# Performance work log

Measured on AMD Instinct MI355X. Metric: run time of the kernel, lower is better.

The kernel has to match this reference:

```python
import jax, jax.numpy as jnp
import numpy as np

B, D, F = 4096, 2048, 16384


def setup_inputs() -> dict:
    key = jax.random.key(0)
    ks = jax.random.split(key, 5)
    s_enc = 1.0 / np.sqrt(D)
    s_dec = 1.0 / np.sqrt(F)
    return {
        "x": jax.random.normal(ks[0], (B, D), dtype=jnp.float32),
        "W_enc": jax.random.normal(ks[1], (F, D), dtype=jnp.float32) * s_enc,
        "b_enc": jnp.zeros((F,), dtype=jnp.float32),
        "W_kest1": jax.random.normal(ks[2], (F, D), dtype=jnp.float32) * s_enc,
        "b_kest1": jnp.zeros((F,), dtype=jnp.float32),
        "W_kest2": jax.random.normal(ks[3], (1, F), dtype=jnp.float32) * s_dec,
        "b_kest2": jnp.zeros((1,), dtype=jnp.float32),
        "W_dec": jax.random.normal(ks[4], (D, F), dtype=jnp.float32) * s_dec,
        "b_dec": jnp.zeros((D,), dtype=jnp.float32),
        "k": 64,
    }


def topk_per_row(acts, k_est):
    # rank of each element when sorted descending (ties resolved stably;
    # after ReLU ties are zeros, so output is identical either way)
    order = jnp.argsort(-acts, axis=1)          # [B, F] descending order
    rank = jnp.argsort(order, axis=1)           # rank[i,j] = position of acts[i,j]
    mask = rank < k_est[:, None]                # per-row dynamic (float) k
    return acts * mask


def reference(x, W_enc, b_enc, W_kest1, b_kest1, W_kest2, b_kest2, W_dec, b_dec, k):
    xc = x - b_dec                                              # [B, D]
    acts = jax.nn.relu(xc @ W_enc.T + b_enc)                    # [B, F]
    h = jax.nn.relu(xc @ W_kest1.T + b_kest1)                   # [B, F]
    k_est = jax.nn.sigmoid(h @ W_kest2.T + b_kest2)[:, 0] * (2.0 * k)  # [B]
    enc = topk_per_row(acts, k_est)                             # [B, F] sparse codes
    x_hat = enc @ W_dec.T + b_dec                               # [B, D]
    return x_hat
```

## Files before the change

kernel.cpp:

```cpp
#include <hip/hip_runtime.h>
#include <hip/hip_bf16.h>
#include <cstdint>
#include <cstddef>

#define BATCH 4096
#define DIM   2048
#define FEAT  16384
#define MAXF  2048

typedef __attribute__((ext_vector_type(8))) _Float16 h8v;
typedef __attribute__((ext_vector_type(4))) float f4v;
typedef __attribute__((ext_vector_type(4))) unsigned short us4v;

__device__ __forceinline__ void split2(float v, unsigned short &h, unsigned short &l){
  _Float16 hf = (_Float16)v;
  _Float16 lf = (_Float16)((v - (float)hf) * 2048.0f);
  h = __builtin_bit_cast(unsigned short, hf);
  l = __builtin_bit_cast(unsigned short, lf);
}

__device__ __forceinline__ void gload16(const void* g, void* l){
  __builtin_amdgcn_global_load_lds(
      (const __attribute__((address_space(1))) void*)g,
      (__attribute__((address_space(3))) void*)l, 16, 0, 0);
}

__global__ __launch_bounds__(256)
void splitX(const float* __restrict__ x, const float* __restrict__ bdec,
            unsigned short* __restrict__ p0, unsigned short* __restrict__ p1)
{
  const size_t i = ((size_t)blockIdx.x * 256 + threadIdx.x) * 4;
  const int col = (int)(i & (DIM - 1));
  const float4 v = *(const float4*)(x + i);
  const float4 b = *(const float4*)(bdec + col);
  float e0 = v.x - b.x, e1 = v.y - b.y, e2 = v.z - b.z, e3 = v.w - b.w;
  ushort4 H, L;
  split2(e0, H.x, L.x); split2(e1, H.y, L.y);
  split2(e2, H.z, L.z); split2(e3, H.w, L.w);
  *(ushort4*)(p0 + i) = H; *(ushort4*)(p1 + i) = L;
}

__global__ __launch_bounds__(256)
void splitW(const float* __restrict__ w,
            unsigned short* __restrict__ p0, unsigned short* __restrict__ p1)
{
  const size_t i = ((size_t)blockIdx.x * 256 + threadIdx.x) * 4;
  const float4 v = *(const float4*)(w + i);
  ushort4 H, L;
  split2(v.x, H.x, L.x); split2(v.y, H.y, L.y);
  split2(v.z, H.z, L.z); split2(v.w, H.w, L.w);
  *(ushort4*)(p0 + i) = H; *(ushort4*)(p1 + i) = L;
}

__global__ __launch_bounds__(256)
void splitW1(const float* __restrict__ w, unsigned short* __restrict__ p0)
{
  const size_t i = ((size_t)blockIdx.x * 256 + threadIdx.x) * 4;
  const float4 v = *(const float4*)(w + i);
  ushort4 H;
  H.x = __builtin_bit_cast(unsigned short, (_Float16)v.x);
  H.y = __builtin_bit_cast(unsigned short, (_Float16)v.y);
  H.z = __builtin_bit_cast(unsigned short, (_Float16)v.z);
  H.w = __builtin_bit_cast(unsigned short, (_Float16)v.w);
  *(ushort4*)(p0 + i) = H;
}

__global__ __launch_bounds__(256, 2)
void gemmd(const unsigned short* __restrict__ Ah_, const unsigned short* __restrict__ B1h_,
           const unsigned short* __restrict__ B2h_,
           const float* __restrict__ benc, const float* __restrict__ bk1,
           const float* __restrict__ w2,
           _Float16* __restrict__ acts16, float* __restrict__ zpart)
{
  __shared__ unsigned short sAB[2][3][128][32];
  const int tid  = threadIdx.x;
  const int lane = tid & 63, wv = tid >> 6;

  const int bid = blockIdx.x;
  const int xcd = bid & 7;
  const int idx = bid >> 3;
  const int sq  = idx >> 6;
  const int s   = idx & 63;
  const int bx  = (xcd << 4) | ((sq & 1) << 3) | (s & 7);
  const int by  = ((sq >> 1) << 3) | (s >> 3);
  const int row0 = by << 7, col0 = bx << 7;

  const int wr = (wv & 1) << 6, wc = (wv >> 1) << 6;

  f4v acc1[4][4], acc2[4][4];
  #pragma unroll
  for (int i = 0; i < 4; ++i)
    #pragma unroll
    for (int j = 0; j < 4; ++j){
      acc1[i][j] = (f4v){0.f, 0.f, 0.f, 0.f};
      acc2[i][j] = (f4v){0.f, 0.f, 0.f, 0.f};
    }

  const unsigned short* gsrc[6];
  unsigned ldsoff[6];
  #pragma unroll
  for (int j = 0; j < 6; ++j){
    const int q = wv * 6 + j;
    const int mat = q >> 3;
    const int chunk = q & 7;
    const int r  = (chunk << 4) + (lane >> 2);
    const int gl = (lane & 3) ^ ((r >> 1) & 3);
    const int rowg = ((mat == 0) ? row0 : col0) + r;
    const unsigned short* P = (mat == 0) ? Ah_ : ((mat == 1) ? B1h_ : B2h_);
    gsrc[j]  = P + (size_t)rowg * DIM + (gl << 3);
    ldsoff[j] = (unsigned)(mat * 8192 + chunk * 1024);
  }

  const int fr16 = lane & 15;
  const int kg   = lane >> 4;
  int ra[4], rb[4];
  #pragma unroll
  for (int f = 0; f < 4; ++f){ ra[f] = wr + (f << 4) + fr16; rb[f] = wc + (f << 4) + fr16; }

  #define LDFRAGD(bf, mat, r) \
    (*(const h8v*)((const char*)sAB + (bf) * 24576 + (mat) * 8192 + (r) * 64 + (((kg ^ (((r) >> 1) & 3)) << 4))))
  #define STAGED(bf, ko)                                                      \
    {                                                                         \
      _Pragma("unroll")                                                       \
      for (int j = 0; j < 6; ++j)                                             \
        gload16(gsrc[j] + (ko), (char*)sAB + (bf) * 24576 + ldsoff[j]);       \
    }

  int cur = 0;
  STAGED(0, 0);
  __syncthreads();

  for (int kt = 0; kt < DIM / 32; ++kt){
    if (kt < DIM / 32 - 1) STAGED(cur ^ 1, (kt + 1) << 5);

    h8v Ahf[4], Bf[4];
    #pragma unroll
    for (int f = 0; f < 4; ++f) Ahf[f] = LDFRAGD(cur, 0, ra[f]);
    #pragma unroll
    for (int f = 0; f < 4; ++f) Bf[f] = LDFRAGD(cur, 1, rb[f]);
    #pragma unroll
    for (int fi = 0; fi < 4; ++fi)
      #pragma unroll
      for (int fj = 0; fj < 4; ++fj)
        acc1[fi][fj] = __builtin_amdgcn_mfma_f32_16x16x32_f16(Bf[fj], Ahf[fi], acc1[fi][fj], 0, 0, 0);
    #pragma unroll
    for (int f = 0; f < 4; ++f) Bf[f] = LDFRAGD(cur, 2, rb[f]);
    #pragma unroll
    for (int fi = 0; fi < 4; ++fi)
      #pragma unroll
      for (int fj = 0; fj < 4; ++fj)
        acc2[fi][fj] = __builtin_amdgcn_mfma_f32_16x16x32_f16(Bf[fj], Ahf[fi], acc2[fi][fj], 0, 0, 0);

    __syncthreads();
    cur ^= 1;
  }
  #undef LDFRAGD
  #undef STAGED

  const int mloc = lane & 15;
  const int nq   = (lane >> 4) << 2;
  #pragma unroll
  for (int fi = 0; fi < 4; ++fi){
    const int grow = row0 + wr + (fi << 4) + mloc;
    #pragma unroll
    for (int fj = 0; fj < 4; ++fj){
      const int gcol = col0 + wc + (fj << 4) + nq;
      const float4 be = *(const float4*)(benc + gcol);
      us4v h;
      h[0] = __builtin_bit_cast(unsigned short, (_Float16)fmaxf(acc1[fi][fj][0] + be.x, 0.f));
      h[1] = __builtin_bit_cast(unsigned short, (_Float16)fmaxf(acc1[fi][fj][1] + be.y, 0.f));
      h[2] = __builtin_bit_cast(unsigned short, (_Float16)fmaxf(acc1[fi][fj][2] + be.z, 0.f));
      h[3] = __builtin_bit_cast(unsigned short, (_Float16)fmaxf(acc1[fi][fj][3] + be.w, 0.f));
      __builtin_nontemporal_store(h, (us4v*)(acts16 + (size_t)grow * FEAT + gcol));
    }
  }
  #pragma unroll
  for (int fi = 0; fi < 4; ++fi){
    float ssum = 0.f;
    #pragma unroll
    for (int fj = 0; fj < 4; ++fj){
      const int gcol = col0 + wc + (fj << 4) + nq;
      const float4 be = *(const float4*)(bk1 + gcol);
      const float4 wk = *(const float4*)(w2 + gcol);
      float h0 = fmaxf(acc2[fi][fj][0] + be.x, 0.f);
      float h1 = fmaxf(acc2[fi][fj][1] + be.y, 0.f);
      float h2 = fmaxf(acc2[fi][fj][2] + be.z, 0.f);
      float h3 = fmaxf(acc2[fi][fj][3] + be.w, 0.f);
      ssum = fmaf(h0, wk.x, ssum);
      ssum = fmaf(h1, wk.y, ssum);
      ssum = fmaf(h2, wk.z, ssum);
      ssum = fmaf(h3, wk.w, ssum);
    }
    ssum += __shfl_xor(ssum, 16);
    ssum += __shfl_xor(ssum, 32);
    if (lane < 16){
      const int grow = row0 + wr + (fi << 4) + lane;
      zpart[(size_t)grow * 256 + (bx << 1) + (wc >> 6)] = ssum;
    }
  }
}

__global__ __launch_bounds__(512, 4)
void gemmx(const unsigned short* __restrict__ Ah_, const unsigned short* __restrict__ Al_,
           const unsigned short* __restrict__ Bh_, const unsigned short* __restrict__ Bl_,
           const float* __restrict__ bias, const float* __restrict__ w2,
           const int* __restrict__ rowList, const int* __restrict__ nflagp,
           float* __restrict__ zexact)
{
  const int panel = blockIdx.x >> 7;
  const int bx    = blockIdx.x & 127;
  const int row0p = panel << 7;
  if (row0p >= *nflagp) return;
  const int col0 = bx << 7;

  __shared__ unsigned short sAB[2][2][128][64];
  const int tid  = threadIdx.x;
  const int lane = tid & 63, wv = tid >> 6;
  const int wr = (wv & 3) << 5, wc = (wv >> 2) << 6;

  f4v acc[2][4], acc2[2][4];
  #pragma unroll
  for (int i = 0; i < 2; ++i)
    #pragma unroll
    for (int j = 0; j < 4; ++j){
      acc[i][j]  = (f4v){0.f, 0.f, 0.f, 0.f};
      acc2[i][j] = (f4v){0.f, 0.f, 0.f, 0.f};
    }

  const unsigned short* gsrc[4];
  unsigned ldsoff[4];
  #pragma unroll
  for (int j = 0; j < 4; ++j){
    const int q = (wv << 2) + j;
    const int mat = q >> 4;
    const int chunk = q & 15;
    const int r  = (chunk << 3) + (lane >> 3);
    const int gl = (lane & 7) ^ (r & 7);
    const int co = (gl & 3) << 3;
    const unsigned short* hi = (mat == 0) ? Ah_ : Bh_;
    const unsigned short* lo = (mat == 0) ? Al_ : Bl_;
    const int rowg = (mat == 0) ? rowList[row0p + r] : (col0 + r);
    gsrc[j]  = ((gl < 4) ? hi : lo) + (size_t)rowg * DIM + co;
    ldsoff[j] = (unsigned)(mat * 16384 + chunk * 1024);
  }

  const int fr16 = lane & 15;
  const int kg   = lane >> 4;
  int ra[2], rb[4];
  #pragma unroll
  for (int f = 0; f < 2; ++f) ra[f] = wr + (f << 4) + fr16;
  #pragma unroll
  for (int f = 0; f < 4; ++f) rb[f] = wc + (f << 4) + fr16;

  #define LDFRAG(bf, mat, r, hb) \
    (*(const h8v*)((const char*)sAB + (bf) * 32768 + (mat) * 16384 + (r) * 128 + (((((hb) + kg) ^ ((r) & 7)) << 4))))
  #define STAGE(bf, ko)                                                       \
    {                                                                         \
      _Pragma("unroll")                                                       \
      for (int j = 0; j < 4; ++j)                                             \
        gload16(gsrc[j] + (ko), (char*)sAB + (bf) * 32768 + ldsoff[j]);       \
    }

  int cur = 0;
  STAGE(0, 0);
  __syncthreads();

  for (int kt = 0; kt < DIM / 32; ++kt){
    if (kt < DIM / 32 - 1) STAGE(cur ^ 1, (kt + 1) << 5);

    h8v Ahf[2], Bhf[4], Xl[4];
    #pragma unroll
    for (int f = 0; f < 2; ++f) Ahf[f] = LDFRAG(cur, 0, ra[f], 0);
    #pragma unroll
    for (int f = 0; f < 4; ++f) Bhf[f] = LDFRAG(cur, 1, rb[f], 0);
    #pragma unroll
    for (int fi = 0; fi < 2; ++fi)
      #pragma unroll
      for (int fj = 0; fj < 4; ++fj)
        acc[fi][fj] = __builtin_amdgcn_mfma_f32_16x16x32_f16(Bhf[fj], Ahf[fi], acc[fi][fj], 0, 0, 0);
    #pragma unroll
    for (int f = 0; f < 2; ++f) Xl[f] = LDFRAG(cur, 0, ra[f], 4);
    #pragma unroll
    for (int fi = 0; fi < 2; ++fi)
      #pragma unroll
      for (int fj = 0; fj < 4; ++fj)
        acc2[fi][fj] = __builtin_amdgcn_mfma_f32_16x16x32_f16(Bhf[fj], Xl[fi], acc2[fi][fj], 0, 0, 0);
    #pragma unroll
    for (int f = 0; f < 4; ++f) Xl[f] = LDFRAG(cur, 1, rb[f], 4);
    #pragma unroll
    for (int fi = 0; fi < 2; ++fi)
      #pragma unroll
      for (int fj = 0; fj < 4; ++fj)
        acc2[fi][fj] = __builtin_amdgcn_mfma_f32_16x16x32_f16(Xl[fj], Ahf[fi], acc2[fi][fj], 0, 0, 0);

    __syncthreads();
    cur ^= 1;
  }
  #undef LDFRAG
  #undef STAGE

  const float LSC = 1.0f / 2048.0f;
  const int nq = (lane >> 4) << 2;
  #pragma unroll
  for (int fi = 0; fi < 2; ++fi){
    float ssum = 0.f;
    #pragma unroll
    for (int fj = 0; fj < 4; ++fj){
      const int gcol = col0 + wc + (fj << 4) + nq;
      const float4 be = *(const float4*)(bias + gcol);
      const float4 wk = *(const float4*)(w2 + gcol);
      float h0 = fmaxf(acc[fi][fj][0] + LSC * acc2[fi][fj][0] + be.x, 0.f);
      float h1 = fmaxf(acc[fi][fj][1] + LSC * acc2[fi][fj][1] + be.y, 0.f);
      float h2 = fmaxf(acc[fi][fj][2] + LSC * acc2[fi][fj][2] + be.z, 0.f);
      float h3 = fmaxf(acc[fi][fj][3] + LSC * acc2[fi][fj][3] + be.w, 0.f);
      ssum = fmaf(h0, wk.x, ssum);
      ssum = fmaf(h1, wk.y, ssum);
      ssum = fmaf(h2, wk.z, ssum);
      ssum = fmaf(h3, wk.w, ssum);
    }
    ssum += __shfl_xor(ssum, 16);
    ssum += __shfl_xor(ssum, 32);
    if (lane < 16){
      const int pos = row0p + wr + (fi << 4) + lane;
      zexact[(size_t)pos * 256 + (bx << 1) + (wc >> 6)] = ssum;
    }
  }
}

__global__ __launch_bounds__(256)
void zinit(int* __restrict__ rowList, int* __restrict__ nflag)
{
  const int i = blockIdx.x * 256 + threadIdx.x;
  if (i < MAXF) rowList[i] = 0;
  if (i == 0) *nflag = 0;
}

__global__ __launch_bounds__(256)
void zreduce_flag(const float* __restrict__ zpart, const float* __restrict__ bk2,
                  const int* __restrict__ kp, int* __restrict__ mrow,
                  int* __restrict__ rowList, int* __restrict__ nflag)
{
  const int row  = blockIdx.x * 4 + (threadIdx.x >> 6);
  const int lane = threadIdx.x & 63;
  const float* zp = zpart + (size_t)row * 256;
  float s = zp[lane] + zp[lane + 64] + zp[lane + 128] + zp[lane + 192];
  s += __shfl_xor(s, 1);
  s += __shfl_xor(s, 2);
  s += __shfl_xor(s, 4);
  s += __shfl_xor(s, 8);
  s += __shfl_xor(s, 16);
  s += __shfl_xor(s, 32);
  if (lane == 0){
    float z = s + bk2[0];
    float kest = 2.f * (float)(*kp) * (1.f / (1.f + expf(-z)));
    int m = (int)ceilf(kest);
    m = min(max(m, 0), 128);
    mrow[row] = m;
    const float frac = kest - floorf(kest);
    const float dmin = fminf(frac, 1.f - frac);
    if (dmin < 0.1f){
      int p = atomicAdd(nflag, 1);
      if (p < MAXF) rowList[p] = row;
    }
  }
}

__global__ __launch_bounds__(256)
void zreduce2(const float* __restrict__ zexact, const int* __restrict__ rowList,
              const int* __restrict__ nflagp, const float* __restrict__ bk2,
              const int* __restrict__ kp, int* __restrict__ mrow)
{
  const int pos  = blockIdx.x * 4 + (threadIdx.x >> 6);
  const int lane = threadIdx.x & 63;
  const int nf = min(*nflagp, MAXF);
  if (pos >= nf) return;
  const float* zp = zexact + (size_t)pos * 256;
  float s = zp[lane] + zp[lane + 64] + zp[lane + 128] + zp[lane + 192];
  s += __shfl_xor(s, 1);
  s += __shfl_xor(s, 2);
  s += __shfl_xor(s, 4);
  s += __shfl_xor(s, 8);
  s += __shfl_xor(s, 16);
  s += __shfl_xor(s, 32);
  if (lane == 0){
    float z = s + bk2[0];
    float kest = 2.f * (float)(*kp) * (1.f / (1.f + expf(-z)));
    int m = (int)ceilf(kest);
    m = min(max(m, 0), 128);
    mrow[rowList[pos]] = m;
  }
}

__device__ __forceinline__ void radix_find(int* hist, int nbins, int need, int tid,
                                           int* out3, int* blksum)
{
  const int per  = nbins >> 8;
  const int base = tid * per;
  int bs = 0;
  for (int j = 0; j < per; ++j) bs += hist[base + j];
  blksum[tid] = bs;
  __syncthreads();
  if (tid == 0){
    int a2 = 0;
    for (int t = 255; t >= 0; --t){ int v = blksum[t]; blksum[t] = a2; a2 += v; }
  }
  __syncthreads();
  int ch = blksum[tid];
  for (int j = per - 1; j >= 0; --j){
    const int b = base + j;
    const int c = hist[b];
    if (ch < need && need <= ch + c){ out3[0] = b; out3[1] = need - ch; out3[2] = ch; }
    ch += c;
  }
  __syncthreads();
}

__global__ __launch_bounds__(256)
void select_band(const _Float16* __restrict__ acts16, const float* __restrict__ x,
                 const float* __restrict__ bdec, const float* __restrict__ Wenc,
                 const int* __restrict__ mrow, int* __restrict__ selIdx,
                 float* __restrict__ selVal, int* __restrict__ scount)
{
  __shared__ int hist[2048];
  __shared__ int blksum[256];
  __shared__ int out3[4];
  __shared__ unsigned short listU[2048];
  __shared__ int listI[2048];
  __shared__ int h32[32];
  __shared__ int lcnt, dcnt, acnt;
  __shared__ unsigned short ambU[64];
  __shared__ int ambI[64];
  __shared__ double ambE[64];
  __shared__ double wred[4];

  const int row = blockIdx.x, tid = threadIdx.x;
  const int m = mrow[row];
  const unsigned short* rp = (const unsigned short*)(acts16 + (size_t)row * FEAT);
  const int base = row << 7;

  for (int i = tid; i < 2048; i += 256) hist[i] = 0;
  __syncthreads();
  for (int it = 0; it < 8; ++it){
    const int i8 = (it << 8) + tid;
    const uint4 u4 = *(const uint4*)(rp + i8 * 8);
    #pragma unroll
    for (int w = 0; w < 4; ++w){
      const unsigned ww = (&u4.x)[w];
      const unsigned a = ww & 0xFFFFu, b = ww >> 16;
      if (a) atomicAdd(&hist[a >> 5], 1);
      if (b) atomicAdd(&hist[b >> 5], 1);
    }
  }
  __syncthreads();
  radix_find(hist, 2048, m, tid, out3, blksum);
  const int bin1 = out3[0];
  const int rem1 = out3[1];
  const int bin1m1 = (bin1 > 1) ? bin1 - 1 : 1;

  if (tid == 0){ lcnt = 0; dcnt = 0; acnt = 0; }
  if (tid < 32) h32[tid] = 0;
  __syncthreads();
  for (int it = 0; it < 8; ++it){
    const int i8 = (it << 8) + tid;
    const uint4 u4 = *(const uint4*)(rp + i8 * 8);
    const int ib = i8 << 3;
    #pragma unroll
    for (int w = 0; w < 4; ++w){
      const unsigned ww = (&u4.x)[w];
      const unsigned a = ww & 0xFFFFu, b = ww >> 16;
      if ((int)(a >> 5) >= bin1m1){
        int p = atomicAdd(&lcnt, 1);
        if (p < 2048){ listU[p] = (unsigned short)a; listI[p] = ib + 2 * w; }
      }
      if ((int)(b >> 5) >= bin1m1){
        int p = atomicAdd(&lcnt, 1);
        if (p < 2048){ listU[p] = (unsigned short)b; listI[p] = ib + 2 * w + 1; }
      }
    }
  }
  __syncthreads();
  const int L = min(lcnt, 2048);

  for (int i = tid; i < L; i += 256){
    const unsigned u = listU[i];
    if ((int)(u >> 5) == bin1) atomicAdd(&h32[u & 31], 1);
  }
  __syncthreads();
  if (tid == 0){
    int c = 0, b3 = 0;
    for (int j = 31; j >= 0; --j){
      c += h32[j];
      if (c >= rem1){ b3 = j; break; }
    }
    out3[3] = b3;
  }
  __syncthreads();
  const unsigned short vm16 = (unsigned short)(((unsigned)bin1 << 5) | (unsigned)out3[3]);
  const float vmf = (float)__builtin_bit_cast(_Float16, vm16);
  const float EPS2 = 0.01f;
  const float lo_cut = vmf - EPS2, hi_cut = vmf + EPS2;

  for (int i = tid; i < L; i += 256){
    const float f = (float)__builtin_bit_cast(_Float16, listU[i]);
    if (f > hi_cut){
      int p = atomicAdd(&dcnt, 1);
      selIdx[base + p] = listI[i];
      selVal[base + p] = f;
    } else if (f >= lo_cut){
      int p = atomicAdd(&acnt, 1);
      if (p < 64){ ambU[p] = listU[i]; ambI[p] = listI[i]; }
    }
  }
  __syncthreads();
  const int D = dcnt;
  const int A = min(acnt, 64);
  int need = m - D;
  if (need < 0) need = 0;
  if (need > A) need = A;

  if (need > 0){
    float* xcs = (float*)hist;
    for (int j = tid; j < DIM; j += 256)
      xcs[j] = x[(size_t)row * DIM + j] - bdec[j];
    __syncthreads();
    const int lane = tid & 63, wv = tid >> 6;
    for (int c = 0; c < A; ++c){
      const float* wrow = Wenc + (size_t)ambI[c] * DIM;
      double sd = 0.0;
      for (int j = tid; j < DIM; j += 256)
        sd += (double)xcs[j] * (double)wrow[j];
      #pragma unroll
      for (int off = 32; off; off >>= 1) sd += __shfl_xor(sd, off);
      if (lane == 0) wred[wv] = sd;
      __syncthreads();
      if (tid == 0) ambE[c] = wred[0] + wred[1] + wred[2] + wred[3];
      __syncthreads();
    }
    if (tid == 0){
      for (int e = 0; e < need; ++e){
        int best = -1;
        for (int c = 0; c < A; ++c){
          if (ambI[c] < 0) continue;
          if (best < 0 || ambE[c] > ambE[best] ||
              (ambE[c] == ambE[best] && ambI[c] < ambI[best])) best = c;
        }
        selIdx[base + D + e] = ambI[best];
        selVal[base + D + e] = (float)__builtin_bit_cast(_Float16, ambU[best]);
        ambI[best] = -1;
      }
    }
  }
  if (tid == 0) scount[row] = D + need;
}

__global__ __launch_bounds__(256)
void transpose_dec(const float* __restrict__ Wd, _Float16* __restrict__ WdT16)
{
  __shared__ float t[64][65];
  const int f0 = blockIdx.x << 6, d0 = blockIdx.y << 6;
  const int tx = threadIdx.x & 15, ty = threadIdx.x >> 4;
  #pragma unroll
  for (int r = 0; r < 4; ++r){
    const int d = ty + (r << 4);
    const float4 v = *(const float4*)(Wd + (size_t)(d0 + d) * FEAT + f0 + (tx << 2));
    t[d][(tx << 2) + 0] = v.x;
    t[d][(tx << 2) + 1] = v.y;
    t[d][(tx << 2) + 2] = v.z;
    t[d][(tx << 2) + 3] = v.w;
  }
  __syncthreads();
  #pragma unroll
  for (int r = 0; r < 4; ++r){
    const int f = ty + (r << 4);
    ushort4 o;
    o.x = __builtin_bit_cast(unsigned short, (_Float16)t[(tx << 2) + 0][f]);
    o.y = __builtin_bit_cast(unsigned short, (_Float16)t[(tx << 2) + 1][f]);
    o.z = __builtin_bit_cast(unsigned short, (_Float16)t[(tx << 2) + 2][f]);
    o.w = __builtin_bit_cast(unsigned short, (_Float16)t[(tx << 2) + 3][f]);
    *(ushort4*)(WdT16 + (size_t)(f0 + f) * DIM + d0 + (tx << 2)) = o;
  }
}

__global__ __launch_bounds__(256)
void decode_k(const _Float16* __restrict__ WdT16, const int* __restrict__ selIdx,
              const float* __restrict__ selVal, const int* __restrict__ scount,
              const float* __restrict__ bdec, float* __restrict__ out)
{
  __shared__ int   sI[128];
  __shared__ float sV[128];
  const int row = blockIdx.x, tid = threadIdx.x;
  const int m = scount[row];
  if (tid < m){
    sI[tid] = selIdx[(row << 7) + tid];
    sV[tid] = selVal[(row << 7) + tid];
  }
  __syncthreads();
  const int d = tid << 3;
  float a[8];
  {
    const float4 b0 = *(const float4*)(bdec + d);
    const float4 b1 = *(const float4*)(bdec + d + 4);
    a[0] = b0.x; a[1] = b0.y; a[2] = b0.z; a[3] = b0.w;
    a[4] = b1.x; a[5] = b1.y; a[6] = b1.z; a[7] = b1.w;
  }
  for (int i = 0; i < m; ++i){
    const float v = sV[i];
    const h8v w = *(const h8v*)(WdT16 + (size_t)sI[i] * DIM + d);
    #pragma unroll
    for (int j = 0; j < 8; ++j)
      a[j] = fmaf(v, (float)w[j], a[j]);
  }
  float4 o0 = {a[0], a[1], a[2], a[3]};
  float4 o1 = {a[4], a[5], a[6], a[7]};
  *(float4*)(out + (size_t)row * DIM + d)     = o0;
  *(float4*)(out + (size_t)row * DIM + d + 4) = o1;
}

extern "C" void kernel_launch(void* const* d_in, const int* in_sizes, int n_in,
                              void* d_out, int out_size, void* d_ws, size_t ws_size,
                              hipStream_t stream)
{
  const float* x    = (const float*)d_in[0];
  const float* Wenc = (const float*)d_in[1];
  const float* benc = (const float*)d_in[2];
  const float* Wk1  = (const float*)d_in[3];
  const float* bk1  = (const float*)d_in[4];
  const float* Wk2  = (const float*)d_in[5];
  const float* bk2  = (const float*)d_in[6];
  const float* Wdec = (const float*)d_in[7];
  const float* bdec = (const float*)d_in[8];
  const int*   kp   = (const int*)d_in[9];
  float* out = (float*)d_out;

  char* ws = (char*)d_ws;
  const size_t XS_BYTES   = (size_t)BATCH * DIM * 2;
  const size_t ACTS_BYTES = (size_t)BATCH * FEAT * 4;
  const size_t WP_BYTES   = (size_t)FEAT * DIM * 2;

  unsigned short* xs0 = (unsigned short*)ws;
  unsigned short* xs1 = (unsigned short*)(ws + XS_BYTES);
  char* p = ws + 2 * XS_BYTES;
  _Float16* acts16 = (_Float16*)p;
  _Float16* WdT16  = (_Float16*)p;
  p += ACTS_BYTES;
  unsigned short* wk0 = (unsigned short*)p;
  unsigned short* wk1 = (unsigned short*)(p + WP_BYTES);
  unsigned short* we0 = (unsigned short*)(p + 2 * WP_BYTES);
  p += 3 * WP_BYTES;
  float* zpart  = (float*)p;               p += 4194304;
  int*   mrow   = (int*)p;                 p += 16384;
  int*   selIdx = (int*)p;                 p += 2097152;
  float* selVal = (float*)p;               p += 2097152;
  int*   scount = (int*)p;                 p += 16384;
  int*   rowList= (int*)p;                 p += MAXF * 4;
  int*   nflag  = (int*)p;                 p += 128;
  float* zexact = (float*)p;               p += (size_t)MAXF * 256 * 4;

  (void)ws_size; (void)in_sizes; (void)n_in; (void)out_size;

  splitX<<<dim3(BATCH * DIM / 1024), dim3(256), 0, stream>>>(x, bdec, xs0, xs1);
  splitW<<<dim3(FEAT * DIM / 1024), dim3(256), 0, stream>>>(Wk1, wk0, wk1);
  splitW1<<<dim3(FEAT * DIM / 1024), dim3(256), 0, stream>>>(Wenc, we0);
  gemmd<<<dim3(4096), dim3(256), 0, stream>>>(xs0, we0, wk0, benc, bk1, Wk2,
                                              acts16, zpart);
  zinit<<<dim3(MAXF / 256), dim3(256), 0, stream>>>(rowList, nflag);
  zreduce_flag<<<dim3(BATCH / 4), dim3(256), 0, stream>>>(zpart, bk2, kp, mrow,
                                                          rowList, nflag);
  gemmx<<<dim3(16 * 128), dim3(512), 0, stream>>>(xs0, xs1, wk0, wk1, bk1, Wk2,
                                                  rowList, nflag, zexact);
  zreduce2<<<dim3(MAXF / 4), dim3(256), 0, stream>>>(zexact, rowList, nflag,
                                                     bk2, kp, mrow);
  select_band<<<dim3(BATCH), dim3(256), 0, stream>>>(acts16, x, bdec, Wenc, mrow,
                                                     selIdx, selVal, scount);
  transpose_dec<<<dim3(FEAT / 64, DIM / 64), dim3(256), 0, stream>>>(Wdec, WdT16);
  decode_k<<<dim3(BATCH), dim3(256), 0, stream>>>(WdT16, selIdx, selVal, scount, bdec, out);
}
```

Baseline: 1.127 ms.

## Split dual-GEMM across 8 waves by role and merge weight split kernels

The fused encoder/k-estimator GEMM now uses 512 threads, with waves 0-3 computing the W_enc tile and waves 4-7 the W_kest1 tile. Each wave holds one accumulator set instead of two, which lowers register pressure per wave and allows three blocks per CU instead of two. The A fragments are now read from LDS by both wave groups, which doubles LDS read traffic for A, and the larger block size may affect scheduling. Separately, the two weight-split kernels are merged into one 2D-grid launch and zinit is moved earlier to cut launch overhead.

```diff
diff --git a/kernel.cpp b/kernel.cpp
--- a/kernel.cpp
+++ b/kernel.cpp
@@ -41,31 +41,29 @@
 }
 
 __global__ __launch_bounds__(256)
-void splitW(const float* __restrict__ w,
-            unsigned short* __restrict__ p0, unsigned short* __restrict__ p1)
+void splitWs(const float* __restrict__ wk1src, const float* __restrict__ wencsrc,
+             unsigned short* __restrict__ wk0, unsigned short* __restrict__ wk1lo,
+             unsigned short* __restrict__ we0)
 {
   const size_t i = ((size_t)blockIdx.x * 256 + threadIdx.x) * 4;
-  const float4 v = *(const float4*)(w + i);
-  ushort4 H, L;
-  split2(v.x, H.x, L.x); split2(v.y, H.y, L.y);
-  split2(v.z, H.z, L.z); split2(v.w, H.w, L.w);
-  *(ushort4*)(p0 + i) = H; *(ushort4*)(p1 + i) = L;
-}
-
-__global__ __launch_bounds__(256)
-void splitW1(const float* __restrict__ w, unsigned short* __restrict__ p0)
-{
-  const size_t i = ((size_t)blockIdx.x * 256 + threadIdx.x) * 4;
-  const float4 v = *(const float4*)(w + i);
-  ushort4 H;
-  H.x = __builtin_bit_cast(unsigned short, (_Float16)v.x);
-  H.y = __builtin_bit_cast(unsigned short, (_Float16)v.y);
-  H.z = __builtin_bit_cast(unsigned short, (_Float16)v.z);
-  H.w = __builtin_bit_cast(unsigned short, (_Float16)v.w);
-  *(ushort4*)(p0 + i) = H;
-}
-
-__global__ __launch_bounds__(256, 2)
+  if (blockIdx.y == 0){
+    const float4 v = *(const float4*)(wk1src + i);
+    ushort4 H, L;
+    split2(v.x, H.x, L.x); split2(v.y, H.y, L.y);
+    split2(v.z, H.z, L.z); split2(v.w, H.w, L.w);
+    *(ushort4*)(wk0 + i) = H; *(ushort4*)(wk1lo + i) = L;
+  } else {
+    const float4 v = *(const float4*)(wencsrc + i);
+    ushort4 H;
+    H.x = __builtin_bit_cast(unsigned short, (_Float16)v.x);
+    H.y = __builtin_bit_cast(unsigned short, (_Float16)v.y);
+    H.z = __builtin_bit_cast(unsigned short, (_Float16)v.z);
+    H.w = __builtin_bit_cast(unsigned short, (_Float16)v.w);
+    *(ushort4*)(we0 + i) = H;
+  }
+}
+
+__global__ __launch_bounds__(512, 3)
 void gemmd(const unsigned short* __restrict__ Ah_, const unsigned short* __restrict__ B1h_,
            const unsigned short* __restrict__ B2h_,
            const float* __restrict__ benc, const float* __restrict__ bk1,
@@ -85,22 +83,22 @@
   const int by  = ((sq >> 1) << 3) | (s >> 3);
   const int row0 = by << 7, col0 = bx << 7;
 
-  const int wr = (wv & 1) << 6, wc = (wv >> 1) << 6;
-
-  f4v acc1[4][4], acc2[4][4];
+  const int role = wv >> 2;
+  const int wloc = wv & 3;
+  const int wr = (wloc & 1) << 6, wc = (wloc >> 1) << 6;
+
+  f4v acc[4][4];
   #pragma unroll
   for (int i = 0; i < 4; ++i)
     #pragma unroll
-    for (int j = 0; j < 4; ++j){
-      acc1[i][j] = (f4v){0.f, 0.f, 0.f, 0.f};
-      acc2[i][j] = (f4v){0.f, 0.f, 0.f, 0.f};
-    }
-
-  const unsigned short* gsrc[6];
-  unsigned ldsoff[6];
-  #pragma unroll
-  for (int j = 0; j < 6; ++j){
-    const int q = wv * 6 + j;
+    for (int j = 0; j < 4; ++j)
+      acc[i][j] = (f4v){0.f, 0.f, 0.f, 0.f};
+
+  const unsigned short* gsrc[3];
+  unsigned ldsoff[3];
+  #pragma unroll
+  for (int j = 0; j < 3; ++j){
+    const int q = wv * 3 + j;
     const int mat = q >> 3;
     const int chunk = q & 7;
     const int r  = (chunk << 4) + (lane >> 2);
@@ -113,6 +111,7 @@
 
   const int fr16 = lane & 15;
   const int kg   = lane >> 4;
+  const int bmat = 1 + role;
   int ra[4], rb[4];
   #pragma unroll
   for (int f = 0; f < 4; ++f){ ra[f] = wr + (f << 4) + fr16; rb[f] = wc + (f << 4) + fr16; }
@@ -122,7 +121,7 @@
   #define STAGED(bf, ko)                                                      \
     {                                                                         \
       _Pragma("unroll")                                                       \
-      for (int j = 0; j < 6; ++j)                                             \
+      for (int j = 0; j < 3; ++j)                                             \
         gload16(gsrc[j] + (ko), (char*)sAB + (bf) * 24576 + ldsoff[j]);       \
     }
 
@@ -133,23 +132,16 @@
   for (int kt = 0; kt < DIM / 32; ++kt){
     if (kt < DIM / 32 - 1) STAGED(cur ^ 1, (kt + 1) << 5);
 
-    h8v Ahf[4], Bf[4];
+    h8v Ahf[4], Bhf[4];
     #pragma unroll
     for (int f = 0; f < 4; ++f) Ahf[f] = LDFRAGD(cur, 0, ra[f]);
     #pragma unroll
-    for (int f = 0; f < 4; ++f) Bf[f] = LDFRAGD(cur, 1, rb[f]);
+    for (int f = 0; f < 4; ++f) Bhf[f] = LDFRAGD(cur, bmat, rb[f]);
     #pragma unroll
     for (int fi = 0; fi < 4; ++fi)
       #pragma unroll
       for (int fj = 0; fj < 4; ++fj)
-        acc1[fi][fj] = __builtin_amdgcn_mfma_f32_16x16x32_f16(Bf[fj], Ahf[fi], acc1[fi][fj], 0, 0, 0);
-    #pragma unroll
-    for (int f = 0; f < 4; ++f) Bf[f] = LDFRAGD(cur, 2, rb[f]);
-    #pragma unroll
-    for (int fi = 0; fi < 4; ++fi)
-      #pragma unroll
-      for (int fj = 0; fj < 4; ++fj)
-        acc2[fi][fj] = __builtin_amdgcn_mfma_f32_16x16x32_f16(Bf[fj], Ahf[fi], acc2[fi][fj], 0, 0, 0);
+        acc[fi][fj] = __builtin_amdgcn_mfma_f32_16x16x32_f16(Bhf[fj], Ahf[fi], acc[fi][fj], 0, 0, 0);
 
     __syncthreads();
     cur ^= 1;
@@ -159,43 +151,46 @@
 
   const int mloc = lane & 15;
   const int nq   = (lane >> 4) << 2;
-  #pragma unroll
-  for (int fi = 0; fi < 4; ++fi){
-    const int grow = row0 + wr + (fi << 4) + mloc;
-    #pragma unroll
-    for (int fj = 0; fj < 4; ++fj){
-      const int gcol = col0 + wc + (fj << 4) + nq;
-      const float4 be = *(const float4*)(benc + gcol);
-      us4v h;
-      h[0] = __builtin_bit_cast(unsigned short, (_Float16)fmaxf(acc1[fi][fj][0] + be.x, 0.f));
-      h[1] = __builtin_bit_cast(unsigned short, (_Float16)fmaxf(acc1[fi][fj][1] + be.y, 0.f));
-      h[2] = __builtin_bit_cast(unsigned short, (_Float16)fmaxf(acc1[fi][fj][2] + be.z, 0.f));
-      h[3] = __builtin_bit_cast(unsigned short, (_Float16)fmaxf(acc1[fi][fj][3] + be.w, 0.f));
-      __builtin_nontemporal_store(h, (us4v*)(acts16 + (size_t)grow * FEAT + gcol));
-    }
-  }
-  #pragma unroll
-  for (int fi = 0; fi < 4; ++fi){
-    float ssum = 0.f;
-    #pragma unroll
-    for (int fj = 0; fj < 4; ++fj){
-      const int gcol = col0 + wc + (fj << 4) + nq;
-      const float4 be = *(const float4*)(bk1 + gcol);
-      const float4 wk = *(const float4*)(w2 + gcol);
-      float h0 = fmaxf(acc2[fi][fj][0] + be.x, 0.f);
-      float h1 = fmaxf(acc2[fi][fj][1] + be.y, 0.f);
-      float h2 = fmaxf(acc2[fi][fj][2] + be.z, 0.f);
-      float h3 = fmaxf(acc2[fi][fj][3] + be.w, 0.f);
-      ssum = fmaf(h0, wk.x, ssum);
-      ssum = fmaf(h1, wk.y, ssum);
-      ssum = fmaf(h2, wk.z, ssum);
-      ssum = fmaf(h3, wk.w, ssum);
-    }
-    ssum += __shfl_xor(ssum, 16);
-    ssum += __shfl_xor(ssum, 32);
-    if (lane < 16){
-      const int grow = row0 + wr + (fi << 4) + lane;
-      zpart[(size_t)grow * 256 + (bx << 1) + (wc >> 6)] = ssum;
+  if (role == 0){
+    #pragma unroll
+    for (int fi = 0; fi < 4; ++fi){
+      const int grow = row0 + wr + (fi << 4) + mloc;
+      #pragma unroll
+      for (int fj = 0; fj < 4; ++fj){
+        const int gcol = col0 + wc + (fj << 4) + nq;
+        const float4 be = *(const float4*)(benc + gcol);
+        us4v h;
+        h[0] = __builtin_bit_cast(unsigned short, (_Float16)fmaxf(acc[fi][fj][0] + be.x, 0.f));
+        h[1] = __builtin_bit_cast(unsigned short, (_Float16)fmaxf(acc[fi][fj][1] + be.y, 0.f));
+        h[2] = __builtin_bit_cast(unsigned short, (_Float16)fmaxf(acc[fi][fj][2] + be.z, 0.f));
+        h[3] = __builtin_bit_cast(unsigned short, (_Float16)fmaxf(acc[fi][fj][3] + be.w, 0.f));
+        __builtin_nontemporal_store(h, (us4v*)(acts16 + (size_t)grow * FEAT + gcol));
+      }
+    }
+  } else {
+    #pragma unroll
+    for (int fi = 0; fi < 4; ++fi){
+      float ssum = 0.f;
+      #pragma unroll
+      for (int fj = 0; fj < 4; ++fj){
+        const int gcol = col0 + wc + (fj << 4) + nq;
+        const float4 be = *(const float4*)(bk1 + gcol);
+        const float4 wk = *(const float4*)(w2 + gcol);
+        float h0 = fmaxf(acc[fi][fj][0] + be.x, 0.f);
+        float h1 = fmaxf(acc[fi][fj][1] + be.y, 0.f);
+        float h2 = fmaxf(acc[fi][fj][2] + be.z, 0.f);
+        float h3 = fmaxf(acc[fi][fj][3] + be.w, 0.f);
+        ssum = fmaf(h0, wk.x, ssum);
+        ssum = fmaf(h1, wk.y, ssum);
+        ssum = fmaf(h2, wk.z, ssum);
+        ssum = fmaf(h3, wk.w, ssum);
+      }
+      ssum += __shfl_xor(ssum, 16);
+      ssum += __shfl_xor(ssum, 32);
+      if (lane < 16){
+        const int grow = row0 + wr + (fi << 4) + lane;
+        zpart[(size_t)grow * 256 + (bx << 1) + (wc >> 6)] = ssum;
+      }
     }
   }
 }
@@ -658,12 +653,11 @@
 
   (void)ws_size; (void)in_sizes; (void)n_in; (void)out_size;
 
+  zinit<<<dim3(MAXF / 256), dim3(256), 0, stream>>>(rowList, nflag);
   splitX<<<dim3(BATCH * DIM / 1024), dim3(256), 0, stream>>>(x, bdec, xs0, xs1);
-  splitW<<<dim3(FEAT * DIM / 1024), dim3(256), 0, stream>>>(Wk1, wk0, wk1);
-  splitW1<<<dim3(FEAT * DIM / 1024), dim3(256), 0, stream>>>(Wenc, we0);
-  gemmd<<<dim3(4096), dim3(256), 0, stream>>>(xs0, we0, wk0, benc, bk1, Wk2,
+  splitWs<<<dim3(FEAT * DIM / 1024, 2), dim3(256), 0, stream>>>(Wk1, Wenc, wk0, wk1, we0);
+  gemmd<<<dim3(4096), dim3(512), 0, stream>>>(xs0, we0, wk0, benc, bk1, Wk2,
                                               acts16, zpart);
-  zinit<<<dim3(MAXF / 256), dim3(256), 0, stream>>>(rowList, nflag);
   zreduce_flag<<<dim3(BATCH / 4), dim3(256), 0, stream>>>(zpart, bk2, kp, mrow,
                                                           rowList, nflag);
   gemmx<<<dim3(16 * 128), dim3(512), 0, stream>>>(xs0, xs1, wk0, wk1, bk1, Wk2,
```

New measurement: 1.119 ms (median of 2 runs). No clear change (-0.7%).
